# Performance work log

Hardware: AMD Instinct MI355X
Metric: run time of the kernel (lower is better)

## Reference

```python
import jax, jax.numpy as jnp
import numpy as np

HEAD_SIZE = 64
N_EMBED = 1024
B, T = 8, 2048


def setup_inputs() -> dict:
    key = jax.random.key(0)
    ks = jax.random.split(key, 7)
    s = lambda fan_in: 1.0 / np.sqrt(fan_in)
    return {
        "x": jax.random.normal(ks[0], (B, T, N_EMBED), dtype=jnp.float32),
        # Linear weights stored as (in, out) so projection is x @ W + b
        "Wk": jax.random.uniform(ks[1], (N_EMBED, HEAD_SIZE), jnp.float32, -s(N_EMBED), s(N_EMBED)),
        "bk": jax.random.uniform(ks[2], (HEAD_SIZE,), jnp.float32, -s(N_EMBED), s(N_EMBED)),
        "Wq": jax.random.uniform(ks[3], (N_EMBED, HEAD_SIZE), jnp.float32, -s(N_EMBED), s(N_EMBED)),
        "bq": jax.random.uniform(ks[4], (HEAD_SIZE,), jnp.float32, -s(N_EMBED), s(N_EMBED)),
        "Wv": jax.random.uniform(ks[5], (N_EMBED, HEAD_SIZE), jnp.float32, -s(N_EMBED), s(N_EMBED)),
        "bv": jax.random.uniform(ks[6], (HEAD_SIZE,), jnp.float32, -s(N_EMBED), s(N_EMBED)),
    }


def reference(x, Wk, bk, Wq, bq, Wv, bv):
    Bb, Tt, C = x.shape
    k = x @ Wk + bk  # [B,T,H]
    q = x @ Wq + bq
    v = x @ Wv + bv
    # NOTE: original computes k @ q^T (keys as rows, queries as cols)
    wei = jnp.einsum("bth,bsh->bts", k, q) * (C ** -0.5)  # [B,T,T]
    causal = jnp.tril(jnp.ones((Tt, Tt), dtype=bool))
    wei = jnp.where(causal, wei, -jnp.inf)
    # softplus instead of softmax; softplus(-inf) = 0, stable via logaddexp
    wei = jnp.logaddexp(wei, 0.0)
    # dropout omitted (eval mode / deterministic reference)
    out = jnp.einsum("bts,bsh->bth", wei, v)  # [B,T,H]
    return out
```

## Files before the change

kernel.cpp:

```cpp
#include <hip/hip_runtime.h>
#include <hip/hip_bf16.h>
#include <stdint.h>

#define HEAD 64
#define CEMB 1024
#define BB 8
#define TSEQ 2048

typedef __attribute__((ext_vector_type(8))) short bf16x8;
typedef __attribute__((ext_vector_type(4))) float f32x4;

__device__ __forceinline__ unsigned short f2bf(float f) {
    union { float f; uint32_t u; } c; c.f = f;
    uint32_t u = c.u + 0x7FFF + ((c.u >> 16) & 1);
    return (unsigned short)(u >> 16);
}
__device__ __forceinline__ ushort4 f4bf(float4 v) {
    ushort4 u; u.x = f2bf(v.x); u.y = f2bf(v.y); u.z = f2bf(v.z); u.w = f2bf(v.w);
    return u;
}

__global__ __launch_bounds__(256) void prep_w(
        const float* __restrict__ Wk, const float* __restrict__ bk,
        const float* __restrict__ Wq, const float* __restrict__ bq,
        const float* __restrict__ Wv, const float* __restrict__ bv,
        unsigned short* __restrict__ WTf, float* __restrict__ biasb) {
    __shared__ float Wl[3][32][64];
    const int kc = blockIdx.x;
    const int tid = threadIdx.x;
    const float* Ws[3] = {Wk, Wq, Wv};
    const int row = tid >> 3, cf = (tid & 7) * 8;
    #pragma unroll
    for (int p = 0; p < 3; p++) {
        const float* W = Ws[p] + (long)(kc * 32 + row) * 64 + cf;
        float4 v0 = *(const float4*)(W);
        float4 v1 = *(const float4*)(W + 4);
        *(float4*)(&Wl[p][row][cf]) = v0;
        *(float4*)(&Wl[p][row][cf + 4]) = v1;
    }
    __syncthreads();
    #pragma unroll
    for (int i = 0; i < 3; i++) {
        int cid = i * 256 + tid;
        int lane = cid & 63;
        int l15 = lane & 15, q4 = lane >> 4;
        int n = (cid >> 6) * 16 + l15;
        int p = n >> 6, col = n & 63;
        float scale = (p == 1) ? 0.03125f : 1.0f;
        unsigned short o[8];
        for (int e = 0; e < 8; e++) o[e] = f2bf(Wl[p][q4 * 8 + e][col] * scale);
        *(int4*)(WTf + (long)kc * 6144 + (long)cid * 8) = *(int4*)o;
    }
    if (kc == 0 && tid < 192) {
        const float* bs[3] = {bk, bq, bv};
        int p = tid >> 6;
        biasb[tid] = bs[p][tid & 63] * ((p == 1) ? 0.03125f : 1.0f);
    }
}

__global__ __launch_bounds__(768) void proj_gemm(
        const float* __restrict__ x, const unsigned short* __restrict__ WTf,
        const float* __restrict__ biasb,
        unsigned short* __restrict__ Kb, unsigned short* __restrict__ Qb,
        unsigned short* __restrict__ VTb) {
    __shared__ __align__(16) unsigned short As[64 * 1032];

    const int tid = threadIdx.x;
    const int lane = tid & 63, w = tid >> 6;
    const int l15 = lane & 15, q4 = lane >> 4;
    const long rowbase = (long)blockIdx.x * 64;
    const float* xg = x + rowbase * CEMB;

    bf16x8 Breg[32];
    {
        const unsigned short* Bg = WTf + w * 512 + (long)lane * 8;
        #pragma unroll
        for (int kc = 0; kc < 32; kc++)
            Breg[kc] = *(const bf16x8*)(Bg + (long)kc * 6144);
    }

    f32x4 z = {0.f, 0.f, 0.f, 0.f};
    f32x4 acc[4];
    #pragma unroll
    for (int m = 0; m < 4; m++) acc[m] = z;

    {
        #pragma unroll
        for (int it = 0; it < 3; it++) {
            int i = it * 768 + tid;
            if (i < 2048) {
                int row = i >> 5, c4 = (i & 31) * 4;
                float4 v = *(const float4*)(xg + row * CEMB + c4);
                *(ushort4*)(As + row * 1032 + c4) = f4bf(v);
            }
        }
    }
    __syncthreads();

    #pragma unroll
    for (int s = 0; s < 8; s++) {
        float4 pf[3];
        if (s < 7) {
            #pragma unroll
            for (int it = 0; it < 3; it++) {
                int i = it * 768 + tid;
                if (i < 2048) {
                    int row = i >> 5, c4 = (i & 31) * 4;
                    pf[it] = *(const float4*)(xg + row * CEMB + (s + 1) * 128 + c4);
                }
            }
        }
        #pragma unroll
        for (int kc = 0; kc < 4; kc++) {
            const int kg = s * 4 + kc;
            #pragma unroll
            for (int m = 0; m < 4; m++) {
                bf16x8 a = *(const bf16x8*)(As + (m * 16 + l15) * 1032 + kg * 32 + q4 * 8);
                acc[m] = __builtin_amdgcn_mfma_f32_16x16x32_bf16(a, Breg[kg], acc[m], 0, 0, 0);
            }
        }
        if (s < 7) {
            #pragma unroll
            for (int it = 0; it < 3; it++) {
                int i = it * 768 + tid;
                if (i < 2048) {
                    int row = i >> 5, c4 = (i & 31) * 4;
                    *(ushort4*)(As + row * 1032 + (s + 1) * 128 + c4) = f4bf(pf[it]);
                }
            }
            __syncthreads();
        }
    }

    const int n = w * 16 + l15;
    const float bias = biasb[n];
    #pragma unroll
    for (int m = 0; m < 4; m++) {
        const long row0 = rowbase + m * 16 + q4 * 4;
        if (n < 128) {
            unsigned short* dst = (n < 64) ? (Kb + row0 * HEAD + n)
                                           : (Qb + row0 * HEAD + (n - 64));
            for (int r = 0; r < 4; r++)
                dst[r * HEAD] = f2bf(acc[m][r] + bias);
        } else {
            const int h = n - 128;
            const long b = row0 >> 11; const int t = (int)(row0 & 2047);
            ushort4 pk;
            pk.x = f2bf(acc[m][0] + bias);
            pk.y = f2bf(acc[m][1] + bias);
            pk.z = f2bf(acc[m][2] + bias);
            pk.w = f2bf(acc[m][3] + bias);
            *(ushort4*)(VTb + b * (HEAD * (long)TSEQ) + (long)h * TSEQ + t) = pk;
        }
    }
}

__global__ __launch_bounds__(256) void attn(
        const unsigned short* __restrict__ Kb, const unsigned short* __restrict__ Qb,
        const unsigned short* __restrict__ VTb, float* __restrict__ out) {
    __shared__ __align__(16) unsigned short Pl[4][2][32 * 40];
    __shared__ __align__(16) float red[3][64 * 36];

    const int tid = threadIdx.x;
    const int lane = tid & 63, w = tid >> 6;
    const int l15 = lane & 15, q4 = lane >> 4;

    const int bid = blockIdx.x;
    const int ti = 63 - (bid >> 3);
    const int b = bid & 7;
    const int t0 = ti * 32;

    const unsigned short* kb  = Kb  + (long)b * TSEQ * HEAD;
    const unsigned short* qb  = Qb  + (long)b * TSEQ * HEAD;
    const unsigned short* vtb = VTb + (long)b * HEAD * TSEQ;

    bf16x8 kf[2][2];
    for (int tt = 0; tt < 2; tt++)
        for (int kk = 0; kk < 2; kk++)
            kf[tt][kk] = *(const bf16x8*)(kb + (t0 + tt * 16 + l15) * HEAD + kk * 32 + q4 * 8);

    f32x4 z = {0.f, 0.f, 0.f, 0.f};
    f32x4 oacc[4][2];
    for (int hh = 0; hh < 4; hh++) for (int tt = 0; tt < 2; tt++) oacc[hh][tt] = z;

    bf16x8 qpf[2][2], vpf[4];
    if (w <= ti) {
        const int s0 = w * 32;
        for (int st2 = 0; st2 < 2; st2++)
            for (int kk = 0; kk < 2; kk++)
                qpf[st2][kk] = *(const bf16x8*)(qb + (s0 + st2 * 16 + l15) * HEAD + kk * 32 + q4 * 8);
        for (int hh = 0; hh < 4; hh++)
            vpf[hh] = *(const bf16x8*)(vtb + (hh * 16 + l15) * (long)TSEQ + s0 + q4 * 8);
    }

    int buf = 0;
    for (int c = w; c <= ti; c += 4) {
        const int s0 = c * 32;
        unsigned short* myP = &Pl[w][buf][0];

        bf16x8 qf[2][2], vf[4];
        for (int st2 = 0; st2 < 2; st2++)
            for (int kk = 0; kk < 2; kk++) qf[st2][kk] = qpf[st2][kk];
        for (int hh = 0; hh < 4; hh++) vf[hh] = vpf[hh];

        if (c + 4 <= ti) {
            const int sn = (c + 4) * 32;
            for (int st2 = 0; st2 < 2; st2++)
                for (int kk = 0; kk < 2; kk++)
                    qpf[st2][kk] = *(const bf16x8*)(qb + (sn + st2 * 16 + l15) * HEAD + kk * 32 + q4 * 8);
            for (int hh = 0; hh < 4; hh++)
                vpf[hh] = *(const bf16x8*)(vtb + (hh * 16 + l15) * (long)TSEQ + sn + q4 * 8);
        }

        f32x4 sc[2][2];
        for (int st2 = 0; st2 < 2; st2++)
            for (int tt = 0; tt < 2; tt++) {
                f32x4 s = z;
                s = __builtin_amdgcn_mfma_f32_16x16x32_bf16(qf[st2][0], kf[tt][0], s, 0, 0, 0);
                s = __builtin_amdgcn_mfma_f32_16x16x32_bf16(qf[st2][1], kf[tt][1], s, 0, 0, 0);
                sc[st2][tt] = s;
            }
        for (int tt = 0; tt < 2; tt++) {
            const int tg = t0 + tt * 16 + l15;
            for (int st2 = 0; st2 < 2; st2++) {
                ushort4 pk;
                unsigned short pv[4];
                for (int r = 0; r < 4; r++) {
                    int sg = s0 + st2 * 16 + q4 * 4 + r;
                    float p = __logf(1.0f + __expf(sc[st2][tt][r]));
                    if (sg > tg) p = 0.0f;
                    pv[r] = f2bf(p);
                }
                pk.x = pv[0]; pk.y = pv[1]; pk.z = pv[2]; pk.w = pv[3];
                *(ushort4*)(myP + (tt * 16 + l15) * 40 + st2 * 16 + q4 * 4) = pk;
            }
        }
        __threadfence_block();
        bf16x8 pf0 = *(const bf16x8*)(myP + l15 * 40 + q4 * 8);
        bf16x8 pf1 = *(const bf16x8*)(myP + (16 + l15) * 40 + q4 * 8);
        for (int hh = 0; hh < 4; hh++) {
            oacc[hh][0] = __builtin_amdgcn_mfma_f32_16x16x32_bf16(vf[hh], pf0, oacc[hh][0], 0, 0, 0);
            oacc[hh][1] = __builtin_amdgcn_mfma_f32_16x16x32_bf16(vf[hh], pf1, oacc[hh][1], 0, 0, 0);
        }
        buf ^= 1;
    }

    if (w > 0) {
        float* r0 = &red[w - 1][lane * 36];
        for (int hh = 0; hh < 4; hh++)
            for (int tt = 0; tt < 2; tt++)
                *(f32x4*)(r0 + (hh * 2 + tt) * 4) = oacc[hh][tt];
    }
    __syncthreads();
    if (w == 0) {
        for (int i = 0; i < 3; i++) {
            const float* r0 = &red[i][lane * 36];
            for (int hh = 0; hh < 4; hh++)
                for (int tt = 0; tt < 2; tt++)
                    oacc[hh][tt] += *(const f32x4*)(r0 + (hh * 2 + tt) * 4);
        }
        for (int tt = 0; tt < 2; tt++) {
            float* ob = out + ((long)b * TSEQ + t0 + tt * 16 + l15) * HEAD + q4 * 4;
            for (int hh = 0; hh < 4; hh++)
                *(f32x4*)(ob + hh * 16) = oacc[hh][tt];
        }
    }
}

extern "C" void kernel_launch(void* const* d_in, const int* in_sizes, int n_in,
                              void* d_out, int out_size, void* d_ws, size_t ws_size,
                              hipStream_t stream) {
    const float* x  = (const float*)d_in[0];
    const float* Wk = (const float*)d_in[1];
    const float* bk = (const float*)d_in[2];
    const float* Wq = (const float*)d_in[3];
    const float* bq = (const float*)d_in[4];
    const float* Wv = (const float*)d_in[5];
    const float* bv = (const float*)d_in[6];
    float* out = (float*)d_out;

    char* ws = (char*)d_ws;
    unsigned short* WTf   = (unsigned short*)(ws);
    float*          biasb = (float*)(ws + 393216);
    unsigned short* Kb    = (unsigned short*)(ws + 524288);
    unsigned short* Qb    = (unsigned short*)(ws + 524288 + 2097152);
    unsigned short* VTb   = (unsigned short*)(ws + 524288 + 4194304);

    prep_w<<<32, 256, 0, stream>>>(Wk, bk, Wq, bq, Wv, bv, WTf, biasb);
    proj_gemm<<<256, 768, 0, stream>>>(x, WTf, biasb, Kb, Qb, VTb);
    attn<<<512, 256, 0, stream>>>(Kb, Qb, VTb, out);
}
```

Before: 146.0 us.

## Double attention waves per block with tree reduction; stage GEMM weights in halves

The attention kernel now uses 8 waves per block, each taking every eighth key chunk. The P staging buffer and the reduction buffer share one shared-memory region, and partial outputs are combined with a three-level tree reduction. The aim is more parallelism per query tile and better latency hiding, at the cost of extra barriers and larger blocks. The projection GEMM loads weight fragments in two halves of 16 registers instead of 32 up front, which reduces register pressure but adds a mid-loop load stall.

After: 142.0 us. -2.8%, faster.

```diff
diff --git a/kernel.cpp b/kernel.cpp
--- a/kernel.cpp
+++ b/kernel.cpp
@@ -70,19 +70,14 @@
     const int l15 = lane & 15, q4 = lane >> 4;
     const long rowbase = (long)blockIdx.x * 64;
     const float* xg = x + rowbase * CEMB;
-
-    bf16x8 Breg[32];
-    {
-        const unsigned short* Bg = WTf + w * 512 + (long)lane * 8;
-        #pragma unroll
-        for (int kc = 0; kc < 32; kc++)
-            Breg[kc] = *(const bf16x8*)(Bg + (long)kc * 6144);
-    }
+    const unsigned short* Bg = WTf + w * 512 + (long)lane * 8;
 
     f32x4 z = {0.f, 0.f, 0.f, 0.f};
     f32x4 acc[4];
     #pragma unroll
     for (int m = 0; m < 4; m++) acc[m] = z;
+
+    bf16x8 Breg[16];
 
     {
         #pragma unroll
@@ -98,37 +93,45 @@
     __syncthreads();
 
     #pragma unroll
-    for (int s = 0; s < 8; s++) {
-        float4 pf[3];
-        if (s < 7) {
+    for (int half = 0; half < 2; half++) {
+        #pragma unroll
+        for (int i = 0; i < 16; i++)
+            Breg[i] = *(const bf16x8*)(Bg + (long)(half * 16 + i) * 6144);
+
+        #pragma unroll
+        for (int ss = 0; ss < 4; ss++) {
+            const int s = half * 4 + ss;
+            float4 pf[3];
+            if (s < 7) {
+                #pragma unroll
+                for (int it = 0; it < 3; it++) {
+                    int i = it * 768 + tid;
+                    if (i < 2048) {
+                        int row = i >> 5, c4 = (i & 31) * 4;
+                        pf[it] = *(const float4*)(xg + row * CEMB + (s + 1) * 128 + c4);
+                    }
+                }
+            }
             #pragma unroll
-            for (int it = 0; it < 3; it++) {
-                int i = it * 768 + tid;
-                if (i < 2048) {
-                    int row = i >> 5, c4 = (i & 31) * 4;
-                    pf[it] = *(const float4*)(xg + row * CEMB + (s + 1) * 128 + c4);
+            for (int kc = 0; kc < 4; kc++) {
+                const int kg = s * 4 + kc;
+                #pragma unroll
+                for (int m = 0; m < 4; m++) {
+                    bf16x8 a = *(const bf16x8*)(As + (m * 16 + l15) * 1032 + kg * 32 + q4 * 8);
+                    acc[m] = __builtin_amdgcn_mfma_f32_16x16x32_bf16(a, Breg[ss * 4 + kc], acc[m], 0, 0, 0);
                 }
             }
-        }
-        #pragma unroll
-        for (int kc = 0; kc < 4; kc++) {
-            const int kg = s * 4 + kc;
-            #pragma unroll
-            for (int m = 0; m < 4; m++) {
-                bf16x8 a = *(const bf16x8*)(As + (m * 16 + l15) * 1032 + kg * 32 + q4 * 8);
-                acc[m] = __builtin_amdgcn_mfma_f32_16x16x32_bf16(a, Breg[kg], acc[m], 0, 0, 0);
-            }
-        }
-        if (s < 7) {
-            #pragma unroll
-            for (int it = 0; it < 3; it++) {
-                int i = it * 768 + tid;
-                if (i < 2048) {
-                    int row = i >> 5, c4 = (i & 31) * 4;
-                    *(ushort4*)(As + row * 1032 + (s + 1) * 128 + c4) = f4bf(pf[it]);
+            if (s < 7) {
+                #pragma unroll
+                for (int it = 0; it < 3; it++) {
+                    int i = it * 768 + tid;
+                    if (i < 2048) {
+                        int row = i >> 5, c4 = (i & 31) * 4;
+                        *(ushort4*)(As + row * 1032 + (s + 1) * 128 + c4) = f4bf(pf[it]);
+                    }
                 }
-            }
-            __syncthreads();
+                __syncthreads();
+            }
         }
     }
 
@@ -155,11 +158,12 @@
     }
 }
 
-__global__ __launch_bounds__(256) void attn(
+__global__ __launch_bounds__(512) void attn(
         const unsigned short* __restrict__ Kb, const unsigned short* __restrict__ Qb,
         const unsigned short* __restrict__ VTb, float* __restrict__ out) {
-    __shared__ __align__(16) unsigned short Pl[4][2][32 * 40];
-    __shared__ __align__(16) float red[3][64 * 36];
+    __shared__ __align__(16) char sm[36864];
+    unsigned short* Pl = (unsigned short*)sm;
+    float* red = (float*)sm;
 
     const int tid = threadIdx.x;
     const int lane = tid & 63, w = tid >> 6;
@@ -193,18 +197,17 @@
             vpf[hh] = *(const bf16x8*)(vtb + (hh * 16 + l15) * (long)TSEQ + s0 + q4 * 8);
     }
 
-    int buf = 0;
-    for (int c = w; c <= ti; c += 4) {
+    unsigned short* myP = Pl + w * 1280;
+    for (int c = w; c <= ti; c += 8) {
         const int s0 = c * 32;
-        unsigned short* myP = &Pl[w][buf][0];
 
         bf16x8 qf[2][2], vf[4];
         for (int st2 = 0; st2 < 2; st2++)
             for (int kk = 0; kk < 2; kk++) qf[st2][kk] = qpf[st2][kk];
         for (int hh = 0; hh < 4; hh++) vf[hh] = vpf[hh];
 
-        if (c + 4 <= ti) {
-            const int sn = (c + 4) * 32;
+        if (c + 8 <= ti) {
+            const int sn = (c + 8) * 32;
             for (int st2 = 0; st2 < 2; st2++)
                 for (int kk = 0; kk < 2; kk++)
                     qpf[st2][kk] = *(const bf16x8*)(qb + (sn + st2 * 16 + l15) * HEAD + kk * 32 + q4 * 8);
@@ -242,23 +245,49 @@
             oacc[hh][0] = __builtin_amdgcn_mfma_f32_16x16x32_bf16(vf[hh], pf0, oacc[hh][0], 0, 0, 0);
             oacc[hh][1] = __builtin_amdgcn_mfma_f32_16x16x32_bf16(vf[hh], pf1, oacc[hh][1], 0, 0, 0);
         }
-        buf ^= 1;
-    }
-
-    if (w > 0) {
-        float* r0 = &red[w - 1][lane * 36];
+    }
+
+    __syncthreads();
+    if (w >= 4) {
+        float* r0 = red + (w - 4) * 2304 + lane * 36;
         for (int hh = 0; hh < 4; hh++)
             for (int tt = 0; tt < 2; tt++)
                 *(f32x4*)(r0 + (hh * 2 + tt) * 4) = oacc[hh][tt];
     }
     __syncthreads();
+    if (w < 4) {
+        const float* r0 = red + w * 2304 + lane * 36;
+        for (int hh = 0; hh < 4; hh++)
+            for (int tt = 0; tt < 2; tt++)
+                oacc[hh][tt] += *(const f32x4*)(r0 + (hh * 2 + tt) * 4);
+    }
+    __syncthreads();
+    if (w == 2 || w == 3) {
+        float* r0 = red + (w - 2) * 2304 + lane * 36;
+        for (int hh = 0; hh < 4; hh++)
+            for (int tt = 0; tt < 2; tt++)
+                *(f32x4*)(r0 + (hh * 2 + tt) * 4) = oacc[hh][tt];
+    }
+    __syncthreads();
+    if (w < 2) {
+        const float* r0 = red + w * 2304 + lane * 36;
+        for (int hh = 0; hh < 4; hh++)
+            for (int tt = 0; tt < 2; tt++)
+                oacc[hh][tt] += *(const f32x4*)(r0 + (hh * 2 + tt) * 4);
+    }
+    __syncthreads();
+    if (w == 1) {
+        float* r0 = red + lane * 36;
+        for (int hh = 0; hh < 4; hh++)
+            for (int tt = 0; tt < 2; tt++)
+                *(f32x4*)(r0 + (hh * 2 + tt) * 4) = oacc[hh][tt];
+    }
+    __syncthreads();
     if (w == 0) {
-        for (int i = 0; i < 3; i++) {
-            const float* r0 = &red[i][lane * 36];
-            for (int hh = 0; hh < 4; hh++)
-                for (int tt = 0; tt < 2; tt++)
-                    oacc[hh][tt] += *(const f32x4*)(r0 + (hh * 2 + tt) * 4);
-        }
+        const float* r0 = red + lane * 36;
+        for (int hh = 0; hh < 4; hh++)
+            for (int tt = 0; tt < 2; tt++)
+                oacc[hh][tt] += *(const f32x4*)(r0 + (hh * 2 + tt) * 4);
         for (int tt = 0; tt < 2; tt++) {
             float* ob = out + ((long)b * TSEQ + t0 + tt * 16 + l15) * HEAD + q4 * 4;
             for (int hh = 0; hh < 4; hh++)
@@ -288,5 +317,5 @@
 
     prep_w<<<32, 256, 0, stream>>>(Wk, bk, Wq, bq, Wv, bv, WTf, biasb);
     proj_gemm<<<256, 768, 0, stream>>>(x, WTf, biasb, Kb, Qb, VTb);
-    attn<<<512, 256, 0, stream>>>(Kb, Qb, VTb, out);
-}
+    attn<<<512, 512, 0, stream>>>(Kb, Qb, VTb, out);
+}
```
